# Kernel tuning notes

Hardware: AMD Instinct MI355X
Metric: run time of the kernel (lower is better)

The kernel has to match this reference:

```python
import jax, jax.numpy as jnp
from jax import lax
import numpy as np
import math

B, LBL, PRED, CIN = 16, 48, 336, 7
L = LBL + PRED
DM, E = 512, 2
DIN, N, DCONV = 2 * DM, 16, 4
DTR = math.ceil(DM / 16)  # 32
TF = 4  # freq='h' time features
EPS = 1e-5


def _ln(x, w, b):
    m = x.mean(-1, keepdims=True)
    v = ((x - m) ** 2).mean(-1, keepdims=True)
    return (x - m) / jnp.sqrt(v + EPS) * w + b


def _silu(x):
    return x * jax.nn.sigmoid(x)


def _token_embed(x, w):
    # Conv1d(c_in, d_model, k=3, padding=1, circular, bias=False). x: (B,L,C), w: (DM,C,3)
    xp = jnp.concatenate([x[:, -1:], x, x[:, :1]], axis=1)  # circular pad along L
    y = lax.conv_general_dilated(xp.transpose(0, 2, 1), w, (1,), 'VALID',
                                 dimension_numbers=('NCH', 'OIH', 'NCH'))
    return y.transpose(0, 2, 1)  # (B,L,DM)


def _selective_scan(u, dt, A, Bm, Cm):
    # u,dt: (B,L,DIN); A: (DIN,N); Bm,Cm: (B,L,N)
    h0 = jnp.zeros((u.shape[0], DIN, N), u.dtype)

    def step(h, inp):
        u_t, dt_t, B_t, C_t = inp  # (B,DIN),(B,DIN),(B,N),(B,N)
        dA = jnp.exp(dt_t[:, :, None] * A)  # (B,DIN,N)
        h = dA * h + (dt_t * u_t)[:, :, None] * B_t[:, None, :]
        y = jnp.einsum('bdn,bn->bd', h, C_t)
        return h, y

    _, ys = lax.scan(step, h0, (u.transpose(1, 0, 2), dt.transpose(1, 0, 2),
                                Bm.transpose(1, 0, 2), Cm.transpose(1, 0, 2)))
    return ys.transpose(1, 0, 2)  # (B,L,DIN)


def _mamba(x, p):
    (in_w, conv_w, conv_b, xproj_w, dtproj_w, dtproj_b, A_log, Dp, out_w) = p
    xz = x @ in_w.T                      # (B,L,2*DIN)
    xin, z = jnp.split(xz, 2, axis=-1)
    # depthwise causal conv1d, kernel DCONV
    xt = jnp.pad(xin.transpose(0, 2, 1), ((0, 0), (0, 0), (DCONV - 1, 0)))
    xc = lax.conv_general_dilated(xt, conv_w, (1,), 'VALID', feature_group_count=DIN,
                                  dimension_numbers=('NCH', 'OIH', 'NCH'))
    xc = _silu((xc + conv_b[None, :, None]).transpose(0, 2, 1))  # (B,L,DIN)
    dbc = xc @ xproj_w.T                 # (B,L,DTR+2N)
    dt_r, Bm, Cm = dbc[..., :DTR], dbc[..., DTR:DTR + N], dbc[..., DTR + N:]
    dt = jax.nn.softplus(dt_r @ dtproj_w.T + dtproj_b)  # (B,L,DIN)
    A = -jnp.exp(A_log)                  # (DIN,N)
    y = _selective_scan(xc, dt, A, Bm, Cm) + xc * Dp
    y = y * _silu(z)
    return y @ out_w.T                   # (B,L,DM)


def _model(x_dec, x_mark_dec, token_w, timef_w, layer_ps, fin_w, fin_b, out_w):
    mean = lax.stop_gradient(x_dec[:, :LBL].mean(1, keepdims=True))
    head = x_dec[:, :LBL] - mean
    std = lax.stop_gradient(jnp.sqrt(head.var(axis=1, keepdims=True) + EPS))
    head = head / std
    xd = jnp.concatenate([head, x_dec[:, LBL:]], axis=1)
    x = _token_embed(xd, token_w) + x_mark_dec @ timef_w.T  # DataEmbedding_wo_pos (eval: no dropout)
    for i in range(E):
        nw, nb = layer_ps[0][i], layer_ps[1][i]
        mp = tuple(layer_ps[j][i] for j in range(2, 11))
        x = x + _mamba(_ln(x, nw, nb), mp)
    x = _ln(x, fin_w, fin_b)
    out = x @ out_w.T
    out = out * std + mean
    return out[:, -PRED:, :]


def setup_inputs() -> dict:
    key = jax.random.key(0)
    ks = jax.random.split(key, 20)
    s = 0.02
    d = {
        'x_enc': jax.random.normal(ks[0], (B, 96, CIN), jnp.float32),
        'x_mark_enc': jax.random.normal(ks[1], (B, 96, TF), jnp.float32),
        'x_dec': jax.random.normal(ks[2], (B, L, CIN), jnp.float32),
        'x_mark_dec': jax.random.normal(ks[3], (B, L, TF), jnp.float32),
        'token_w': jax.random.normal(ks[4], (DM, CIN, 3), jnp.float32) * s,
        'timef_w': jax.random.normal(ks[5], (DM, TF), jnp.float32) * s,
        'norm_w': jnp.ones((E, DM), jnp.float32),
        'norm_b': jnp.zeros((E, DM), jnp.float32),
        'in_proj_w': jax.random.normal(ks[6], (E, 2 * DIN, DM), jnp.float32) * s,
        'conv_w': jax.random.normal(ks[7], (E, DIN, 1, DCONV), jnp.float32) * s,
        'conv_b': jnp.zeros((E, DIN), jnp.float32),
        'xproj_w': jax.random.normal(ks[8], (E, DTR + 2 * N, DIN), jnp.float32) * s,
        'dtproj_w': jax.random.normal(ks[9], (E, DIN, DTR), jnp.float32) * s,
        'dtproj_b': jnp.full((E, DIN), -4.0, jnp.float32),
        'A_log': jnp.tile(jnp.log(jnp.arange(1, N + 1, dtype=jnp.float32)), (E, DIN, 1)),
        'D': jnp.ones((E, DIN), jnp.float32),
        'outproj_w': jax.random.normal(ks[10], (E, DM, DIN), jnp.float32) * s,
        'final_norm_w': jnp.ones((DM,), jnp.float32),
        'final_norm_b': jnp.zeros((DM,), jnp.float32),
        'out_w': jax.random.normal(ks[11], (CIN, DM), jnp.float32) * s,
    }
    return d


def reference(x_enc, x_mark_enc, x_dec, x_mark_dec, token_w, timef_w, norm_w, norm_b,
              in_proj_w, conv_w, conv_b, xproj_w, dtproj_w, dtproj_b, A_log, D,
              outproj_w, final_norm_w, final_norm_b, out_w):
    layer_ps = (norm_w, norm_b, in_proj_w, conv_w, conv_b, xproj_w, dtproj_w,
                dtproj_b, A_log, D, outproj_w)
    return _model(x_dec, x_mark_dec, token_w, timef_w, layer_ps,
                  final_norm_w, final_norm_b, out_w)
```

## Files before the change

kernel.cpp:

```cpp
#include <hip/hip_runtime.h>

#define B_    16
#define LBL_  48
#define PRED_ 336
#define CIN_  7
#define L_    384
#define DM_   512
#define E_    2
#define DIN_  1024
#define N_    16
#define DCONV_ 4
#define DTR_  32
#define TF_   4
#define EPSF  1e-5f
#define NSEG  16
#define SEGL  24
#define SC2   2
#define NCHK  12

typedef unsigned short u16;
typedef __attribute__((ext_vector_type(8))) short short8;
typedef __attribute__((ext_vector_type(4))) float f32x4;

__device__ __forceinline__ float bf2f(u16 u){
  union { float f; unsigned int i; } cv; cv.i = ((unsigned int)u) << 16; return cv.f;
}
__device__ __forceinline__ u16 f2bf(float f){
  union { float f; unsigned int i; } cv; cv.f = f;
  unsigned int x = cv.i;
  unsigned int lsb = (x >> 16) & 1u;
  x += 0x7fffu + lsb;
  return (u16)(x >> 16);
}
__device__ __forceinline__ float lo16(unsigned int v){
  union { float f; unsigned int i; } cv; cv.i = v << 16; return cv.f;
}
__device__ __forceinline__ float hi16(unsigned int v){
  union { float f; unsigned int i; } cv; cv.i = v & 0xffff0000u; return cv.f;
}

#define GLDS(g, l) __builtin_amdgcn_global_load_lds( \
    (const __attribute__((address_space(1))) void*)(g), \
    (__attribute__((address_space(3))) void*)(l), 16, 0, 0)

#define PO_XDEC   0
#define PO_XMARK  43008
#define PO_TOKW   67584
#define PO_TIMEF  78336
#define PO_NORMW  80384
#define PO_NORMB  81408
#define PO_INW    82432
#define PO_CONVW  2179584
#define PO_CONVB  2187776
#define PO_XPROJ  2189824
#define PO_DTW    2320896
#define PO_DTB    2386432
#define PO_ALOG   2388480
#define PO_DP     2421248
#define PO_OUTW   2423296
#define PO_FNW    3471872
#define PO_FNB    3472384
#define PO_HEADW  3472896
#define P_TOTAL   3476480
#define A_X    3476480
#define A_LNB  6622208
#define A_XZ   9767936
#define A_DT   22350848
#define A_DBC  28642304
#define A_XD   29035520
#define A_MEAN 29078528
#define A_STD  29078640
#define A_DTR  29100032

struct Ptrs { const void* p[18]; };

__device__ __forceinline__ float wredsum(float s){
  #pragma unroll
  for (int off = 32; off; off >>= 1) s += __shfl_xor(s, off, 64);
  return s;
}

__device__ __forceinline__ void qpowers(float q, float* p){
  float q2 = q*q;
  float q4 = q2*q2;
  float q8 = q4*q4;
  float q3 = q2*q;
  p[0]=q;      p[1]=q2;     p[2]=q3;     p[3]=q4;
  p[4]=q4*q;   p[5]=q4*q2;  p[6]=q4*q3;  p[7]=q8;
  p[8]=q8*q;   p[9]=q8*q2;  p[10]=q8*q3; p[11]=q8*q4;
  p[12]=q8*p[4]; p[13]=q8*p[5]; p[14]=q8*p[6]; p[15]=q8*q8;
}

__global__ __launch_bounds__(256) void convert_kernel(Ptrs ps, float* __restrict__ dst){
  const int offs[18] = {PO_XDEC, PO_XMARK, PO_TOKW, PO_TIMEF, PO_NORMW, PO_NORMB,
                        PO_INW, PO_CONVW, PO_CONVB, PO_XPROJ, PO_DTW, PO_DTB,
                        PO_ALOG, PO_DP, PO_OUTW, PO_FNW, PO_FNB, PO_HEADW};
  int idx = blockIdx.x * 256 + threadIdx.x;
  if (idx >= P_TOTAL) return;
  int seg = 0;
  #pragma unroll
  for (int s = 1; s < 18; s++) if (idx >= offs[s]) seg = s;
  int off = idx - offs[seg];
  int isbf = (((const u16*)ps.p[4])[0] == 0x3F80u);
  if (seg == 6 || seg == 9 || seg == 10 || seg == 14){
    u16 hv = isbf ? ((const u16*)ps.p[seg])[off]
                  : f2bf(((const float*)ps.p[seg])[off]);
    ((u16*)(dst + offs[seg]))[off] = hv;
  } else {
    float v = isbf ? bf2f(((const u16*)ps.p[seg])[off])
                   : ((const float*)ps.p[seg])[off];
    dst[idx] = v;
  }
}

__global__ __launch_bounds__(64) void prep_kernel(const float* __restrict__ x_dec, float* __restrict__ xd,
                            float* __restrict__ meanv, float* __restrict__ stdv){
  int i = blockIdx.x;
  int b = i / CIN_, c = i % CIN_;
  int lane = threadIdx.x;
  float v0 = (lane < LBL_) ? x_dec[(b*L_+lane)*CIN_+c] : 0.f;
  float m = wredsum(v0) * (1.f/LBL_);
  float dv = (lane < LBL_) ? (v0 - m) : 0.f;
  float sd = sqrtf(wredsum(dv*dv) * (1.f/LBL_) + EPSF);
  if (lane == 0){ meanv[i] = m; stdv[i] = sd; }
  float inv = 1.f / sd;
  #pragma unroll
  for (int t = lane; t < L_; t += 64){
    float v = x_dec[(b*L_+t)*CIN_+c];
    xd[(b*L_+t)*CIN_+c] = (t < LBL_) ? (v - m) * inv : v;
  }
}

__global__ __launch_bounds__(256) void embed_ln_kernel(const float* __restrict__ xd,
      const float* __restrict__ token_w, const float* __restrict__ x_mark,
      const float* __restrict__ timef_w, const float* __restrict__ nw,
      const float* __restrict__ nb, float* __restrict__ x, u16* __restrict__ out){
  int tok = blockIdx.x*4 + (threadIdx.x >> 6);
  int lane = threadIdx.x & 63;
  int t = tok % L_;
  int b = tok / L_;
  int tm1 = (t == 0) ? L_-1 : t-1;
  int tp1 = (t == L_-1) ? 0 : t+1;
  const float* r0 = xd + (b*L_+tm1)*CIN_;
  const float* r1 = xd + (b*L_+t  )*CIN_;
  const float* r2 = xd + (b*L_+tp1)*CIN_;
  const float* mk = x_mark + (b*L_+t)*TF_;
  float a0[CIN_], a1[CIN_], a2[CIN_], mkv[TF_];
  #pragma unroll
  for (int ci = 0; ci < CIN_; ci++){ a0[ci]=r0[ci]; a1[ci]=r1[ci]; a2[ci]=r2[ci]; }
  #pragma unroll
  for (int f = 0; f < TF_; f++) mkv[f] = mk[f];
  float v[8];
  #pragma unroll
  for (int j = 0; j < 8; j++){
    int d = lane*8 + j;
    float acc = 0.f;
    #pragma unroll
    for (int ci = 0; ci < CIN_; ci++){
      const float* w = token_w + (d*CIN_+ci)*3;
      acc += a0[ci]*w[0] + a1[ci]*w[1] + a2[ci]*w[2];
    }
    #pragma unroll
    for (int f = 0; f < TF_; f++)
      acc += mkv[f] * timef_w[d*TF_+f];
    v[j] = acc;
  }
  float* xr = x + (size_t)tok*DM_ + lane*8;
  *(float4*)xr       = (float4){v[0],v[1],v[2],v[3]};
  *(float4*)(xr + 4) = (float4){v[4],v[5],v[6],v[7]};
  float s = (v[0]+v[1])+(v[2]+v[3])+((v[4]+v[5])+(v[6]+v[7]));
  float mean = wredsum(s) * (1.f/DM_);
  float s2 = 0.f;
  #pragma unroll
  for (int j = 0; j < 8; j++){ v[j] -= mean; s2 += v[j]*v[j]; }
  float rstd = rsqrtf(wredsum(s2) * (1.f/DM_) + EPSF);
  const float* wr = nw + lane*8;
  const float* br = nb + lane*8;
  uint4 o; unsigned int* op = (unsigned int*)&o;
  #pragma unroll
  for (int k = 0; k < 4; k++){
    u16 e0 = f2bf(v[2*k]   * rstd * wr[2*k]   + br[2*k]);
    u16 e1 = f2bf(v[2*k+1] * rstd * wr[2*k+1] + br[2*k+1]);
    op[k] = (unsigned int)e0 | ((unsigned int)e1 << 16);
  }
  *(uint4*)(out + (size_t)tok*DM_ + lane*8) = o;
}

__global__ __launch_bounds__(256) void ln_kernel(const float* __restrict__ x,
     const float* __restrict__ w, const float* __restrict__ bias, u16* __restrict__ out){
  int tok = blockIdx.x*4 + (threadIdx.x >> 6);
  int lane = threadIdx.x & 63;
  const float* xr = x + (size_t)tok*DM_ + lane*8;
  float4 a = *(const float4*)xr;
  float4 bq = *(const float4*)(xr + 4);
  float v[8] = {a.x,a.y,a.z,a.w,bq.x,bq.y,bq.z,bq.w};
  float s = (v[0]+v[1])+(v[2]+v[3])+((v[4]+v[5])+(v[6]+v[7]));
  float mean = wredsum(s) * (1.f/DM_);
  float s2 = 0.f;
  #pragma unroll
  for (int j = 0; j < 8; j++){ v[j] -= mean; s2 += v[j]*v[j]; }
  float rstd = rsqrtf(wredsum(s2) * (1.f/DM_) + EPSF);
  const float* wr = w + lane*8;
  const float* br = bias + lane*8;
  uint4 o; unsigned int* op = (unsigned int*)&o;
  #pragma unroll
  for (int k = 0; k < 4; k++){
    u16 e0 = f2bf(v[2*k]   * rstd * wr[2*k]   + br[2*k]);
    u16 e1 = f2bf(v[2*k+1] * rstd * wr[2*k+1] + br[2*k+1]);
    op[k] = (unsigned int)e0 | ((unsigned int)e1 << 16);
  }
  *(uint4*)(out + (size_t)tok*DM_ + lane*8) = o;
}

template<int TN, int ACCUM, int BF16OUT, int DTR>
__global__ __launch_bounds__(256) void gemm_mfma(const u16* __restrict__ A, const u16* __restrict__ Wt,
    void* __restrict__ C, int M, int N, int K, u16* __restrict__ dtrb){
  constexpr int WN = TN / 2;
  constexpr int NI = WN / 16;
  __shared__ u16 As[128 * 32];
  __shared__ u16 Ws[TN * 32];
  int tid = threadIdx.x;
  int wv = tid >> 6, lane = tid & 63;
  int wm = (wv & 1) * 64, wn = (wv >> 1) * WN;
  int m0 = blockIdx.y * 128, n0 = blockIdx.x * TN;
  int la = lane & 15, lk = lane >> 4;
  f32x4 acc[4][NI];
  #pragma unroll
  for (int i = 0; i < 4; i++)
    #pragma unroll
    for (int j = 0; j < NI; j++) acc[i][j] = (f32x4){0.f, 0.f, 0.f, 0.f};
  int srow = lane >> 2, scol = (lane & 3) * 8;
  const u16* Ag0 = A + (size_t)(m0 + wv*32 + srow) * K + scol;
  const u16* Ag1 = Ag0 + (size_t)16 * K;
  u16* Al0 = As + wv*1024 + lane*8;
  u16* Al1 = As + wv*1024 + 512 + lane*8;
  const u16 *Wg0, *Wg1;
  u16 *Wl0, *Wl1;
  if constexpr (TN == 128){
    Wg0 = Wt + (size_t)(n0 + wv*32 + srow) * K + scol;
    Wg1 = Wg0 + (size_t)16 * K;
    Wl0 = Ws + wv*1024 + lane*8;
    Wl1 = Ws + wv*1024 + 512 + lane*8;
  } else {
    Wg0 = Wt + (size_t)(n0 + wv*16 + srow) * K + scol;
    Wg1 = nullptr;
    Wl0 = Ws + wv*512 + lane*8;
    Wl1 = nullptr;
  }
  for (int k0 = 0; k0 < K; k0 += 32){
    GLDS(Ag0 + k0, Al0);
    GLDS(Ag1 + k0, Al1);
    GLDS(Wg0 + k0, Wl0);
    if constexpr (TN == 128) GLDS(Wg1 + k0, Wl1);
    __syncthreads();
    short8 af[4], bfr[NI];
    #pragma unroll
    for (int mi = 0; mi < 4; mi++) af[mi] = *(const short8*)&As[(wm + mi*16 + la)*32 + lk*8];
    #pragma unroll
    for (int ni = 0; ni < NI; ni++) bfr[ni] = *(const short8*)&Ws[(wn + ni*16 + la)*32 + lk*8];
    #pragma unroll
    for (int mi = 0; mi < 4; mi++)
      #pragma unroll
      for (int ni = 0; ni < NI; ni++)
        acc[mi][ni] = __builtin_amdgcn_mfma_f32_16x16x32_bf16(af[mi], bfr[ni], acc[mi][ni], 0, 0, 0);
    __syncthreads();
  }
  #pragma unroll
  for (int mi = 0; mi < 4; mi++)
    #pragma unroll
    for (int ni = 0; ni < NI; ni++){
      int row = m0 + wm + mi*16 + lk*4;
      int col = n0 + wn + ni*16 + la;
      #pragma unroll
      for (int r = 0; r < 4; r++){
        if constexpr (BF16OUT){
          u16* p = (u16*)C + (size_t)row * N + col;
          p[(size_t)r * N] = f2bf(acc[mi][ni][r]);
        } else {
          float* p = (float*)C + (size_t)row * N + col;
          if (ACCUM) p[(size_t)r * N] += acc[mi][ni][r];
          else       p[(size_t)r * N]  = acc[mi][ni][r];
        }
      }
    }
  if constexpr (DTR){
    if (wn == 0){
      #pragma unroll
      for (int mi = 0; mi < 4; mi++)
        #pragma unroll
        for (int ni = 0; ni < NI; ni++){
          int row = m0 + wm + mi*16 + lk*4;
          int col = ni*16 + la;
          #pragma unroll
          for (int r = 0; r < 4; r++)
            dtrb[(size_t)(row + r)*32 + col] = f2bf(acc[mi][ni][r]);
        }
    }
  }
}

__global__ __launch_bounds__(256) void dtproj_mfma(const u16* __restrict__ dtrb,
    const u16* __restrict__ dtwb, const float* __restrict__ dtb, u16* __restrict__ dt){
  __shared__ u16 As[128 * 32];
  __shared__ u16 Ws[64 * 32];
  int tid = threadIdx.x;
  int wv = tid >> 6, lane = tid & 63;
  int wm = (wv & 1) * 64, wn = (wv >> 1) * 32;
  int m0 = blockIdx.y * 128, n0 = blockIdx.x * 64;
  int la = lane & 15, lk = lane >> 4;
  int srow = lane >> 2, scol = (lane & 3) * 8;
  GLDS(dtrb + (size_t)(m0 + wv*32 + srow)*32 + scol,      As + wv*1024 + lane*8);
  GLDS(dtrb + (size_t)(m0 + wv*32 + 16 + srow)*32 + scol, As + wv*1024 + 512 + lane*8);
  GLDS(dtwb + (size_t)(n0 + wv*16 + srow)*32 + scol,      Ws + wv*512 + lane*8);
  __syncthreads();
  short8 af[4], bfr[2];
  #pragma unroll
  for (int mi = 0; mi < 4; mi++) af[mi] = *(const short8*)&As[(wm + mi*16 + la)*32 + lk*8];
  #pragma unroll
  for (int ni = 0; ni < 2; ni++) bfr[ni] = *(const short8*)&Ws[(wn + ni*16 + la)*32 + lk*8];
  #pragma unroll
  for (int mi = 0; mi < 4; mi++)
    #pragma unroll
    for (int ni = 0; ni < 2; ni++){
      f32x4 acc = (f32x4){0.f,0.f,0.f,0.f};
      acc = __builtin_amdgcn_mfma_f32_16x16x32_bf16(af[mi], bfr[ni], acc, 0, 0, 0);
      int row = m0 + wm + mi*16 + lk*4;
      int d   = n0 + wn + ni*16 + la;
      float bias = dtb[d];
      #pragma unroll
      for (int r = 0; r < 4; r++){
        float raw = acc[r] + bias;
        float sp = (raw > 20.f) ? raw : log1pf(__expf(raw));
        dt[(size_t)(row + r)*DIN_ + d] = f2bf(sp);
      }
    }
}

__global__ __launch_bounds__(256) void conv_silu_kernel(const u16* __restrict__ xz,
   const float* __restrict__ cw, const float* __restrict__ cb, u16* __restrict__ xcb){
  int e = blockIdx.x * 256 + threadIdx.x;
  int c8 = (e & (DIN_/8 - 1)) * 8;
  int bt = e >> 7;
  int t  = bt % L_;
  const u16* base = xz + (size_t)bt * (2*DIN_) + c8;
  uint4 tap[4];
  tap[3] = *(const uint4*)base;
  if (t >= 1) tap[2] = *(const uint4*)(base - 1*2*DIN_);
  if (t >= 2) tap[1] = *(const uint4*)(base - 2*2*DIN_);
  if (t >= 3) tap[0] = *(const uint4*)(base - 3*2*DIN_);
  float v[8];
  #pragma unroll
  for (int k = 0; k < 8; k++){
    float4 w = *(const float4*)(cw + (c8 + k)*4);
    float s = cb[c8 + k];
    #pragma unroll
    for (int j = 0; j < 4; j++){
      if (j >= 3 - t){
        const unsigned int* tp = (const unsigned int*)&tap[j];
        float xv = (k & 1) ? hi16(tp[k >> 1]) : lo16(tp[k >> 1]);
        s += xv * ((const float*)&w)[j];
      }
    }
    v[k] = s / (1.f + __expf(-s));
  }
  uint4 o;
  unsigned int* op = (unsigned int*)&o;
  #pragma unroll
  for (int k = 0; k < 4; k++)
    op[k] = (unsigned int)f2bf(v[2*k]) | ((unsigned int)f2bf(v[2*k+1]) << 16);
  *(uint4*)(xcb + (size_t)bt * DIN_ + c8) = o;
}

#define WSTR2 896
__global__ __launch_bounds__(1024, 1) void scan_kernel(
    u16* __restrict__ ub_yb,
    const float* __restrict__ dbc, const u16* __restrict__ xz,
    const u16* __restrict__ dtp,
    const float* __restrict__ A_log, const float* __restrict__ Dp){
  __shared__ float smem[16384];

  int tid = threadIdx.x;
  int lane = tid & 63;
  int seg  = tid >> 6;
  int b = blockIdx.x >> 4;
  int g = blockIdx.x & 15;
  int d = g*64 + lane;
  size_t base = (size_t)b * L_;

  float* wbase = smem + seg * WSTR2;
  float* sbc = wbase;
  float* su  = wbase + 128;
  float* sz  = wbase + 384;
  float* sdt = wbase + 640;

  int st = lane >> 5;
  int j  = lane & 31;

  float A[16];
  #pragma unroll
  for (int n = 0; n < 16; n += 4){
    float4 av = *(const float4*)(A_log + (size_t)d*N_ + n);
    A[n] = -__expf(av.x); A[n+1] = -__expf(av.y); A[n+2] = -__expf(av.z); A[n+3] = -__expf(av.w);
  }
  float Dv = Dp[d];
  bool fastA = true;
  #pragma unroll
  for (int n = 0; n < 16; n++) fastA = fastA && (fabsf(A[n] + (float)(n+1)) < 1e-3f*(n+1));

  float h[16];
  #pragma unroll
  for (int n = 0; n < 16; n++) h[n] = 0.f;

  auto ldc = [&](int c, float& kbc, unsigned int& ku, unsigned int& kz,
                 unsigned int& kt, bool wz){
    size_t tokr = base + seg*SEGL + c*SC2 + st;
    kbc = dbc[tokr*64 + 32 + j];
    ku  = ((const unsigned int*)(ub_yb + tokr*DIN_ + g*64))[j];
    kt  = ((const unsigned int*)(dtp + tokr*DIN_ + g*64))[j];
    if (wz) kz = ((const unsigned int*)(xz + tokr*(2*DIN_) + DIN_ + g*64))[j];
  };
  auto stc = [&](int buf, float kbc, unsigned int ku, unsigned int kz,
                 unsigned int kt, bool wz){
    sbc[buf*64 + st*32 + j] = kbc;
    su [buf*128 + st*64 + 2*j]     = lo16(ku);
    su [buf*128 + st*64 + 2*j + 1] = hi16(ku);
    sdt[buf*128 + st*64 + 2*j]     = lo16(kt);
    sdt[buf*128 + st*64 + 2*j + 1] = hi16(kt);
    if (wz){
      sz[buf*128 + st*64 + 2*j]     = lo16(kz);
      sz[buf*128 + st*64 + 2*j + 1] = hi16(kz);
    }
  };

  float S = 0.f;
  {
    float kbc; unsigned int ku, kz, kt;
    ldc(0, kbc, ku, kz, kt, false);
    stc(0, kbc, ku, kz, kt, false);
    for (int c = 0; c < NCHK; c++){
      int cur = c & 1;
      bool have = (c + 1 < NCHK);
      float nbc; unsigned int nu, nz, nt;
      if (have) ldc(c+1, nbc, nu, nz, nt, false);
      for (int s = 0; s < SC2; s++){
        float dtv = sdt[cur*128 + s*64 + lane];
        float u   = su [cur*128 + s*64 + lane];
        const float* bcrow = sbc + cur*64 + s*32;
        float Bf[16];
        #pragma unroll
        for (int i = 0; i < 16; i += 4){
          float4 bv = *(const float4*)(bcrow + i);
          Bf[i] = bv.x; Bf[i+1] = bv.y; Bf[i+2] = bv.z; Bf[i+3] = bv.w;
        }
        float du = dtv * u;
        S += dtv;
        if (fastA){
          float q = __expf(-dtv);
          float p[16];
          qpowers(q, p);
          #pragma unroll
          for (int n = 0; n < 16; n++) h[n] = p[n] * h[n] + du * Bf[n];
        } else {
          #pragma unroll
          for (int n = 0; n < 16; n++){
            float dA = __expf(dtv * A[n]);
            h[n] = dA * h[n] + du * Bf[n];
          }
        }
      }
      if (have) stc(1 - cur, nbc, nu, nz, nt, false);
    }
  }

  #pragma unroll
  for (int half = 0; half < 2; half++){
    __syncthreads();
    #pragma unroll
    for (int n = 0; n < 8; n++){
      int nn = half*8 + n;
      smem[(n*NSEG + seg)*64 + lane]        = h[nn];
      smem[8192 + (n*NSEG + seg)*64 + lane] = __expf(A[nn] * S);
    }
    __syncthreads();
    float hs[8];
    #pragma unroll
    for (int n = 0; n < 8; n++) hs[n] = 0.f;
    for (int jj = 0; jj < seg; jj++){
      #pragma unroll
      for (int n = 0; n < 8; n++){
        float qh = smem[(n*NSEG + jj)*64 + lane];
        float qP = smem[8192 + (n*NSEG + jj)*64 + lane];
        hs[n] = qh + qP * hs[n];
      }
    }
    #pragma unroll
    for (int n = 0; n < 8; n++) h[half*8 + n] = hs[n];
  }
  __syncthreads();

  {
    float kbc; unsigned int ku, kz, kt;
    ldc(0, kbc, ku, kz, kt, true);
    stc(0, kbc, ku, kz, kt, true);
    for (int c = 0; c < NCHK; c++){
      int cur = c & 1;
      bool have = (c + 1 < NCHK);
      float nbc; unsigned int nu, nz, nt;
      if (have) ldc(c+1, nbc, nu, nz, nt, true);
      for (int s = 0; s < SC2; s++){
        float dtv = sdt[cur*128 + s*64 + lane];
        float u   = su [cur*128 + s*64 + lane];
        float z   = sz [cur*128 + s*64 + lane];
        const float* bcrow = sbc + cur*64 + s*32;
        float Bf[16], Cf[16];
        #pragma unroll
        for (int i = 0; i < 16; i += 4){
          float4 bv = *(const float4*)(bcrow + i);
          float4 cv = *(const float4*)(bcrow + 16 + i);
          Bf[i] = bv.x; Bf[i+1] = bv.y; Bf[i+2] = bv.z; Bf[i+3] = bv.w;
          Cf[i] = cv.x; Cf[i+1] = cv.y; Cf[i+2] = cv.z; Cf[i+3] = cv.w;
        }
        float du = dtv * u;
        float acc = 0.f;
        if (fastA){
          float q = __expf(-dtv);
          float p[16];
          qpowers(q, p);
          #pragma unroll
          for (int n = 0; n < 16; n++){
            h[n] = p[n] * h[n] + du * Bf[n];
            acc += h[n] * Cf[n];
          }
        } else {
          #pragma unroll
          for (int n = 0; n < 16; n++){
            float dA = __expf(dtv * A[n]);
            h[n] = dA * h[n] + du * Bf[n];
            acc += h[n] * Cf[n];
          }
        }
        float y = acc + u * Dv;
        size_t tok = base + seg*SEGL + c*SC2 + s;
        ub_yb[tok*DIN_ + d] = f2bf(y * (z / (1.f + __expf(-z))));
      }
      if (have) stc(1 - cur, nbc, nu, nz, nt, true);
    }
  }
}

__global__ __launch_bounds__(256) void head_kernel(const float* __restrict__ x,
    const float* __restrict__ fw, const float* __restrict__ fb, const float* __restrict__ ow,
    const float* __restrict__ meanv, const float* __restrict__ stdv, void* __restrict__ out,
    const u16* __restrict__ dtype_probe){
  int wav = blockIdx.x*4 + (threadIdx.x >> 6);
  int lane = threadIdx.x & 63;
  if (wav >= B_*PRED_) return;
  int b = wav / PRED_;
  int tt = wav % PRED_;
  int tok = b*L_ + LBL_ + tt;
  const float* xr = x + (size_t)tok*DM_ + lane*8;
  float4 a = *(const float4*)xr;
  float4 bq = *(const float4*)(xr + 4);
  float v[8] = {a.x,a.y,a.z,a.w,bq.x,bq.y,bq.z,bq.w};
  float s = (v[0]+v[1])+(v[2]+v[3])+((v[4]+v[5])+(v[6]+v[7]));
  float mean = wredsum(s) * (1.f/DM_);
  float s2 = 0.f;
  #pragma unroll
  for (int j = 0; j < 8; j++){ v[j] -= mean; s2 += v[j]*v[j]; }
  float rstd = rsqrtf(wredsum(s2) * (1.f/DM_) + EPSF);
  const float* fwr = fw + lane*8;
  const float* fbr = fb + lane*8;
  #pragma unroll
  for (int j = 0; j < 8; j++) v[j] = v[j] * rstd * fwr[j] + fbr[j];
  int isbf = (dtype_probe[0] == 0x3F80u);
  for (int o = 0; o < CIN_; o++){
    const float* owr = ow + (size_t)o*DM_ + lane*8;
    float part = 0.f;
    #pragma unroll
    for (int j = 0; j < 8; j++) part += v[j] * owr[j];
    part = wredsum(part);
    if (lane == 0){
      float res = part * stdv[b*CIN_ + o] + meanv[b*CIN_ + o];
      size_t oidx = (size_t)(b*PRED_ + tt)*CIN_ + o;
      if (isbf) ((u16*)out)[oidx] = f2bf(res);
      else      ((float*)out)[oidx] = res;
    }
  }
}

extern "C" void kernel_launch(void* const* d_in, const int* in_sizes, int n_in,
                              void* d_out, int out_size, void* d_ws, size_t ws_size,
                              hipStream_t stream){
  float* P = (float*)d_ws;

  Ptrs ps;
  for (int i = 0; i < 18; i++) ps.p[i] = d_in[2 + i];

  float* x    = P + A_X;
  u16*   lnxb = (u16*)(P + A_LNB);
  u16*   xcb  = (u16*)(P + A_LNB);
  u16*   xz   = (u16*)(P + A_XZ);
  u16*   dt   = (u16*)(P + A_DT);
  u16*   dtrb = (u16*)(P + A_DTR);
  float* dbc  = P + A_DBC;
  float* xd   = P + A_XD;
  float* meanv= P + A_MEAN;
  float* stdv = P + A_STD;
  const u16* bwi = (const u16*)(P + PO_INW);
  const u16* bwx = (const u16*)(P + PO_XPROJ);
  const u16* bwd = (const u16*)(P + PO_DTW);
  const u16* bwo = (const u16*)(P + PO_OUTW);

  convert_kernel<<<(P_TOTAL+255)/256, 256, 0, stream>>>(ps, P);
  prep_kernel<<<B_*CIN_, 64, 0, stream>>>(P + PO_XDEC, xd, meanv, stdv);
  embed_ln_kernel<<<(B_*L_)/4, 256, 0, stream>>>(
      xd, P + PO_TOKW, P + PO_XMARK, P + PO_TIMEF,
      P + PO_NORMW, P + PO_NORMB, x, lnxb);

  for (int e = 0; e < E_; e++){
    if (e > 0)
      ln_kernel<<<(B_*L_)/4, 256, 0, stream>>>(x, P + PO_NORMW + e*DM_, P + PO_NORMB + e*DM_, lnxb);
    gemm_mfma<128,0,1,0><<<dim3((2*DIN_)/128, (B_*L_)/128), 256, 0, stream>>>(
        lnxb, bwi + (size_t)e*2*DIN_*DM_, xz, B_*L_, 2*DIN_, DM_, nullptr);
    conv_silu_kernel<<<(B_*L_*DIN_)/(256*8), 256, 0, stream>>>(
        xz, P + PO_CONVW + e*DIN_*DCONV_, P + PO_CONVB + e*DIN_, xcb);
    gemm_mfma<64,0,0,1><<<dim3(1, (B_*L_)/128), 256, 0, stream>>>(
        xcb, bwx + (size_t)e*64*DIN_, dbc, B_*L_, 64, DIN_, dtrb);
    dtproj_mfma<<<dim3(DIN_/64, (B_*L_)/128), 256, 0, stream>>>(
        dtrb, bwd + (size_t)e*DIN_*DTR_, P + PO_DTB + e*DIN_, dt);
    scan_kernel<<<256, 1024, 0, stream>>>(
        xcb, dbc, xz, dt, P + PO_ALOG + e*DIN_*N_, P + PO_DP + e*DIN_);
    gemm_mfma<64,1,0,0><<<dim3(DM_/64, (B_*L_)/128), 256, 0, stream>>>(
        xcb, bwo + (size_t)e*DM_*DIN_, x, B_*L_, DM_, DIN_, nullptr);
  }

  head_kernel<<<(B_*PRED_+3)/4, 256, 0, stream>>>(
      x, P + PO_FNW, P + PO_FNB, P + PO_HEADW, meanv, stdv, d_out, (const u16*)d_in[6]);
}
```

Baseline: 451.0 us.

## Fuse input normalization into embedding and double GEMM K-tile to 64

Removes the separate prep kernel: each embedding wave recomputes the per-channel mean and std over the label window directly from the raw decoder input and normalizes on the fly, saving one launch and an intermediate buffer. Separately, the bf16 MFMA GEMM now stages 64-wide K tiles in shared memory and runs two MFMA sub-steps per tile, halving the number of barrier pairs per K loop at the cost of doubled LDS use. The fused embed kernel repeats the statistics reductions in every block, which is redundant work but small.

```diff
diff --git a/kernel.cpp b/kernel.cpp
--- a/kernel.cpp
+++ b/kernel.cpp
@@ -67,7 +67,6 @@
 #define A_XZ   9767936
 #define A_DT   22350848
 #define A_DBC  28642304
-#define A_XD   29035520
 #define A_MEAN 29078528
 #define A_STD  29078640
 #define A_DTR  29100032
@@ -113,43 +112,53 @@
   }
 }
 
-__global__ __launch_bounds__(64) void prep_kernel(const float* __restrict__ x_dec, float* __restrict__ xd,
-                            float* __restrict__ meanv, float* __restrict__ stdv){
-  int i = blockIdx.x;
-  int b = i / CIN_, c = i % CIN_;
-  int lane = threadIdx.x;
-  float v0 = (lane < LBL_) ? x_dec[(b*L_+lane)*CIN_+c] : 0.f;
-  float m = wredsum(v0) * (1.f/LBL_);
-  float dv = (lane < LBL_) ? (v0 - m) : 0.f;
-  float sd = sqrtf(wredsum(dv*dv) * (1.f/LBL_) + EPSF);
-  if (lane == 0){ meanv[i] = m; stdv[i] = sd; }
-  float inv = 1.f / sd;
-  #pragma unroll
-  for (int t = lane; t < L_; t += 64){
-    float v = x_dec[(b*L_+t)*CIN_+c];
-    xd[(b*L_+t)*CIN_+c] = (t < LBL_) ? (v - m) * inv : v;
-  }
-}
-
-__global__ __launch_bounds__(256) void embed_ln_kernel(const float* __restrict__ xd,
+__global__ __launch_bounds__(256) void embed_ln_kernel(const void* __restrict__ xdec,
+      const u16* __restrict__ dtype_probe,
       const float* __restrict__ token_w, const float* __restrict__ x_mark,
       const float* __restrict__ timef_w, const float* __restrict__ nw,
-      const float* __restrict__ nb, float* __restrict__ x, u16* __restrict__ out){
+      const float* __restrict__ nb, float* __restrict__ x, u16* __restrict__ out,
+      float* __restrict__ meanv, float* __restrict__ stdv){
+  int isbf = (dtype_probe[0] == 0x3F80u);
   int tok = blockIdx.x*4 + (threadIdx.x >> 6);
   int lane = threadIdx.x & 63;
   int t = tok % L_;
   int b = tok / L_;
+  float xv[CIN_];
+  #pragma unroll
+  for (int c = 0; c < CIN_; c++){
+    float v = 0.f;
+    if (lane < LBL_)
+      v = isbf ? bf2f(((const u16*)xdec)[(b*L_+lane)*CIN_+c])
+               : ((const float*)xdec)[(b*L_+lane)*CIN_+c];
+    xv[c] = v;
+  }
+  float m[CIN_], inv[CIN_], sd[CIN_];
+  #pragma unroll
+  for (int c = 0; c < CIN_; c++){
+    float mm = wredsum(xv[c]) * (1.f/LBL_);
+    float dv = (lane < LBL_) ? (xv[c] - mm) : 0.f;
+    float vv = wredsum(dv*dv) * (1.f/LBL_);
+    float s = sqrtf(vv + EPSF);
+    m[c] = mm; sd[c] = s; inv[c] = 1.f/s;
+  }
+  if (lane == 0){
+    #pragma unroll
+    for (int c = 0; c < CIN_; c++){ meanv[b*CIN_+c] = m[c]; stdv[b*CIN_+c] = sd[c]; }
+  }
   int tm1 = (t == 0) ? L_-1 : t-1;
   int tp1 = (t == L_-1) ? 0 : t+1;
-  const float* r0 = xd + (b*L_+tm1)*CIN_;
-  const float* r1 = xd + (b*L_+t  )*CIN_;
-  const float* r2 = xd + (b*L_+tp1)*CIN_;
-  const float* mk = x_mark + (b*L_+t)*TF_;
   float a0[CIN_], a1[CIN_], a2[CIN_], mkv[TF_];
   #pragma unroll
-  for (int ci = 0; ci < CIN_; ci++){ a0[ci]=r0[ci]; a1[ci]=r1[ci]; a2[ci]=r2[ci]; }
-  #pragma unroll
-  for (int f = 0; f < TF_; f++) mkv[f] = mk[f];
+  for (int c = 0; c < CIN_; c++){
+    float v0 = isbf ? bf2f(((const u16*)xdec)[(b*L_+tm1)*CIN_+c]) : ((const float*)xdec)[(b*L_+tm1)*CIN_+c];
+    float v1 = isbf ? bf2f(((const u16*)xdec)[(b*L_+t  )*CIN_+c]) : ((const float*)xdec)[(b*L_+t  )*CIN_+c];
+    float v2 = isbf ? bf2f(((const u16*)xdec)[(b*L_+tp1)*CIN_+c]) : ((const float*)xdec)[(b*L_+tp1)*CIN_+c];
+    a0[c] = (tm1 < LBL_) ? (v0 - m[c]) * inv[c] : v0;
+    a1[c] = (t   < LBL_) ? (v1 - m[c]) * inv[c] : v1;
+    a2[c] = (tp1 < LBL_) ? (v2 - m[c]) * inv[c] : v2;
+  }
+  #pragma unroll
+  for (int f = 0; f < TF_; f++) mkv[f] = x_mark[(b*L_+t)*TF_+f];
   float v[8];
   #pragma unroll
   for (int j = 0; j < 8; j++){
@@ -217,8 +226,8 @@
     void* __restrict__ C, int M, int N, int K, u16* __restrict__ dtrb){
   constexpr int WN = TN / 2;
   constexpr int NI = WN / 16;
-  __shared__ u16 As[128 * 32];
-  __shared__ u16 Ws[TN * 32];
+  __shared__ u16 As[128 * 64];
+  __shared__ u16 Ws[TN * 64];
   int tid = threadIdx.x;
   int wv = tid >> 6, lane = tid & 63;
   int wm = (wv & 1) * 64, wn = (wv >> 1) * WN;
@@ -229,40 +238,42 @@
   for (int i = 0; i < 4; i++)
     #pragma unroll
     for (int j = 0; j < NI; j++) acc[i][j] = (f32x4){0.f, 0.f, 0.f, 0.f};
-  int srow = lane >> 2, scol = (lane & 3) * 8;
-  const u16* Ag0 = A + (size_t)(m0 + wv*32 + srow) * K + scol;
-  const u16* Ag1 = Ag0 + (size_t)16 * K;
-  u16* Al0 = As + wv*1024 + lane*8;
-  u16* Al1 = As + wv*1024 + 512 + lane*8;
-  const u16 *Wg0, *Wg1;
-  u16 *Wl0, *Wl1;
+  int srow = lane >> 3, scol = (lane & 7) * 8;
+  const u16* Ag = A + (size_t)(m0 + wv*32 + srow) * K + scol;
+  u16* Al = As + wv*2048 + lane*8;
+  const u16* Wg;
+  u16* Wl;
   if constexpr (TN == 128){
-    Wg0 = Wt + (size_t)(n0 + wv*32 + srow) * K + scol;
-    Wg1 = Wg0 + (size_t)16 * K;
-    Wl0 = Ws + wv*1024 + lane*8;
-    Wl1 = Ws + wv*1024 + 512 + lane*8;
+    Wg = Wt + (size_t)(n0 + wv*32 + srow) * K + scol;
+    Wl = Ws + wv*2048 + lane*8;
   } else {
-    Wg0 = Wt + (size_t)(n0 + wv*16 + srow) * K + scol;
-    Wg1 = nullptr;
-    Wl0 = Ws + wv*512 + lane*8;
-    Wl1 = nullptr;
-  }
-  for (int k0 = 0; k0 < K; k0 += 32){
-    GLDS(Ag0 + k0, Al0);
-    GLDS(Ag1 + k0, Al1);
-    GLDS(Wg0 + k0, Wl0);
-    if constexpr (TN == 128) GLDS(Wg1 + k0, Wl1);
+    Wg = Wt + (size_t)(n0 + wv*16 + srow) * K + scol;
+    Wl = Ws + wv*1024 + lane*8;
+  }
+  for (int k0 = 0; k0 < K; k0 += 64){
+    #pragma unroll
+    for (int i = 0; i < 4; i++) GLDS(Ag + k0 + (size_t)i*8*K, Al + i*512);
+    if constexpr (TN == 128){
+      #pragma unroll
+      for (int i = 0; i < 4; i++) GLDS(Wg + k0 + (size_t)i*8*K, Wl + i*512);
+    } else {
+      #pragma unroll
+      for (int i = 0; i < 2; i++) GLDS(Wg + k0 + (size_t)i*8*K, Wl + i*512);
+    }
     __syncthreads();
-    short8 af[4], bfr[NI];
-    #pragma unroll
-    for (int mi = 0; mi < 4; mi++) af[mi] = *(const short8*)&As[(wm + mi*16 + la)*32 + lk*8];
-    #pragma unroll
-    for (int ni = 0; ni < NI; ni++) bfr[ni] = *(const short8*)&Ws[(wn + ni*16 + la)*32 + lk*8];
-    #pragma unroll
-    for (int mi = 0; mi < 4; mi++)
-      #pragma unroll
-      for (int ni = 0; ni < NI; ni++)
-        acc[mi][ni] = __builtin_amdgcn_mfma_f32_16x16x32_bf16(af[mi], bfr[ni], acc[mi][ni], 0, 0, 0);
+    #pragma unroll
+    for (int ks = 0; ks < 2; ks++){
+      short8 af[4], bfr[NI];
+      #pragma unroll
+      for (int mi = 0; mi < 4; mi++) af[mi] = *(const short8*)&As[(wm + mi*16 + la)*64 + ks*32 + lk*8];
+      #pragma unroll
+      for (int ni = 0; ni < NI; ni++) bfr[ni] = *(const short8*)&Ws[(wn + ni*16 + la)*64 + ks*32 + lk*8];
+      #pragma unroll
+      for (int mi = 0; mi < 4; mi++)
+        #pragma unroll
+        for (int ni = 0; ni < NI; ni++)
+          acc[mi][ni] = __builtin_amdgcn_mfma_f32_16x16x32_bf16(af[mi], bfr[ni], acc[mi][ni], 0, 0, 0);
+    }
     __syncthreads();
   }
   #pragma unroll
@@ -603,19 +614,18 @@
   u16*   dt   = (u16*)(P + A_DT);
   u16*   dtrb = (u16*)(P + A_DTR);
   float* dbc  = P + A_DBC;
-  float* xd   = P + A_XD;
   float* meanv= P + A_MEAN;
   float* stdv = P + A_STD;
   const u16* bwi = (const u16*)(P + PO_INW);
   const u16* bwx = (const u16*)(P + PO_XPROJ);
   const u16* bwd = (const u16*)(P + PO_DTW);
   const u16* bwo = (const u16*)(P + PO_OUTW);
+  const u16* probe = (const u16*)d_in[6];
 
   convert_kernel<<<(P_TOTAL+255)/256, 256, 0, stream>>>(ps, P);
-  prep_kernel<<<B_*CIN_, 64, 0, stream>>>(P + PO_XDEC, xd, meanv, stdv);
   embed_ln_kernel<<<(B_*L_)/4, 256, 0, stream>>>(
-      xd, P + PO_TOKW, P + PO_XMARK, P + PO_TIMEF,
-      P + PO_NORMW, P + PO_NORMB, x, lnxb);
+      d_in[2], probe, P + PO_TOKW, P + PO_XMARK, P + PO_TIMEF,
+      P + PO_NORMW, P + PO_NORMB, x, lnxb, meanv, stdv);
 
   for (int e = 0; e < E_; e++){
     if (e > 0)
@@ -635,5 +645,5 @@
   }
 
   head_kernel<<<(B_*PRED_+3)/4, 256, 0, stream>>>(
-      x, P + PO_FNW, P + PO_FNB, P + PO_HEADW, meanv, stdv, d_out, (const u16*)d_in[6]);
-}
+      x, P + PO_FNW, P + PO_FNB, P + PO_HEADW, meanv, stdv, d_out, probe);
+}
```

Result: no change. 457.4 us (median of 2 runs) (+1.4%).
